# Kernel optimization log

Hardware: AMD Instinct MI355X
Metric: run time of the kernel (lower is better)

The kernel has to match this reference:

```python
import jax, jax.numpy as jnp
import numpy as np

CASCADES = 3
D, H, W = 64, 256, 256
HID = 8  # BasicBlock hidden channels


def fdiff(x, axis):
    """Forward difference D x along `axis` (last entry 0) == sparse dx/dy/dz matmul."""
    axis = axis % x.ndim
    pad = [(0, 0)] * x.ndim
    pad[axis] = (0, 1)
    return jnp.pad(jnp.diff(x, axis=axis), pad)


def fdiff_t(y, axis):
    """Exact transpose D^T y of fdiff: (D^T y)_0=-y_0, (D^T y)_j=y_{j-1}-y_j, (D^T y)_{n-1}=y_{n-2}."""
    axis = axis % y.ndim
    n = y.shape[axis]
    yl = jax.lax.slice_in_dim(y, 0, n - 1, axis=axis)  # y[0..n-2]
    pf = [(0, 0)] * y.ndim; pf[axis] = (1, 0)
    pb = [(0, 0)] * y.ndim; pb[axis] = (0, 1)
    return jnp.pad(yl, pf) - jnp.pad(yl, pb)


def conv3d(x, w, b):
    out = jax.lax.conv_general_dilated(
        x, w, window_strides=(1, 1, 1), padding='SAME',
        dimension_numbers=('NCDHW', 'OIDHW', 'NCDHW'))
    return out + b[None, :, None, None, None]


def basic_block(x, w1, b1, w2, b2):
    h = jax.nn.relu(conv3d(x, w1, b1))
    return conv3d(h, w2, b2), jnp.mean(jnp.abs(h))


def ite(t, sino):
    """BeijingGeometry stand-in: one SIRT-style step A^T(sino - A t)/D, A = sum over depth."""
    proj = jnp.sum(t, axis=2)               # [B,1,H,W]
    res = sino - proj
    return jnp.broadcast_to(res[:, :, None], t.shape) / t.shape[2]


def setup_inputs() -> dict:
    key = jax.random.key(0)
    ks = jax.random.split(key, 8)
    image = jax.random.normal(ks[0], (1, 1, D, H, W), dtype=jnp.float32)
    sino = jax.random.normal(ks[1], (1, 1, H, W), dtype=jnp.float32)
    # 4 BasicBlocks stacked on leading axis
    W1 = jax.random.normal(ks[2], (4, HID, 1, 3, 3, 3), dtype=jnp.float32) * 0.1
    B1 = jnp.zeros((4, HID), dtype=jnp.float32)
    W2 = jax.random.normal(ks[3], (4, 1, HID, 3, 3, 3), dtype=jnp.float32) * 0.1
    B2 = jnp.zeros((4, 1), dtype=jnp.float32)
    ntx = jnp.full((CASCADES,), -0.01, dtype=jnp.float32)
    nty = jnp.full((CASCADES,), -0.01, dtype=jnp.float32)
    ntz = jnp.full((CASCADES,), -0.01, dtype=jnp.float32)
    nt = jnp.full((CASCADES,), -0.1, dtype=jnp.float32)
    return {"image": image, "sino": sino, "W1": W1, "B1": B1, "W2": W2, "B2": B2,
            "ntx": ntx, "nty": nty, "ntz": ntz, "nt": nt}


def reference(image, sino, W1, B1, W2, B2, ntx, nty, ntz, nt):
    t = image
    p = q = s = jnp.float32(0.0)
    outs = [image]
    for c in range(CASCADES):
        z = t + ite(t, sino)
        pnew, _ = basic_block(fdiff(z, -1), W1[0], B1[0], W2[0], B2[0])  # d/dx (W axis)
        qnew, _ = basic_block(fdiff(z, -2), W1[1], B1[1], W2[1], B2[1])  # d/dy (H axis)
        snew, _ = basic_block(fdiff(z, -3), W1[2], B1[2], W2[2], B2[2])  # d/dz (D axis)
        znew, _ = basic_block(z, W1[3], B1[3], W2[3], B2[3])
        p = p + ntx[c] * (p - pnew)
        q = q + nty[c] * (q - qnew)
        s = s + ntz[c] * (s - snew)
        z_ = t + nt[c] * (t - znew)
        t = fdiff_t(p, -1) + fdiff_t(q, -2) + fdiff_t(s, -3) + z_
        outs.append(t)
    return jnp.stack(outs, axis=0)  # [cascades+1, B, 1, D, H, W]
```

## Files before the change

kernel.cpp:

```cpp
#include <hip/hip_runtime.h>

#define DD 64
#define HH 256
#define WW 256
#define HW (HH * WW)
#define NVOX (DD * HW)

#define TS 32
#define DR 36
#define HPH 40
#define CHB 16
#define NPF 6

typedef __fp16 half2v __attribute__((ext_vector_type(2)));

__global__ __launch_bounds__(256) void k_corr(const float* __restrict__ t,
                                              const float* __restrict__ sino,
                                              float* __restrict__ corr) {
  int idx = blockIdx.x * 256 + threadIdx.x;
  float s = 0.f;
#pragma unroll 8
  for (int d = 0; d < DD; ++d) s += t[d * HW + idx];
  corr[idx] = (sino[idx] - s) * (1.0f / DD);
}

__global__ __launch_bounds__(256, 4) void k_blocks(
    const float* __restrict__ t, const float* __restrict__ corr,
    float* __restrict__ p, float* __restrict__ q, float* __restrict__ s_,
    float* __restrict__ zb,
    const float* __restrict__ W1g, const float* __restrict__ B1g,
    const float* __restrict__ W2g, const float* __restrict__ B2g,
    const float* __restrict__ ntx, const float* __restrict__ nty,
    const float* __restrict__ ntz, const float* __restrict__ nt, int c) {
  __shared__ __align__(16) float dbuf[3][DR][DR];
  __shared__ __align__(16) __fp16 hbuf[8][34][HPH];

  const int b = blockIdx.z & 3;
  const int D0 = (blockIdx.z >> 2) * CHB;
  const int Dend = (D0 + CHB < DD) ? (D0 + CHB) : DD;
  const int ty0 = blockIdx.y * TS;
  const int tx0 = blockIdx.x * TS;
  const int tid = threadIdx.x;

  const float* w1 = W1g + b * 216;
  const float* w2 = W2g + b * 216;
  float b1[8];
#pragma unroll
  for (int ch = 0; ch < 8; ++ch) b1[ch] = B1g[b * 8 + ch];
  const float b2 = B2g[b];
  const float coef = (b == 0) ? ntx[c] : (b == 1) ? nty[c] : (b == 2) ? ntz[c] : nt[c];
  const float* prevBuf = (b == 0) ? p : (b == 1) ? q : (b == 2) ? s_ : t;
  float* outBuf = (b == 0) ? p : (b == 1) ? q : (b == 2) ? s_ : zb;
  const bool zeroPrev = (c == 0) && (b < 3);
  const int strideA = (b == 0) ? 1 : (b == 1) ? WW : HW;

  auto dslot = [](int f) { return (f + 6) % 3; };

  int cbt[NPF];
  float dC[NPF];
  unsigned mbits = 0;
#pragma unroll
  for (int k = 0; k < NPF; ++k) {
    int i = tid + k * 256;
    int iy = i / DR, ix = i - iy * DR;
    int gy = ty0 - 2 + iy, gx = tx0 - 2 + ix;
    bool inb = (i < DR * DR) && ((unsigned)gy < HH) && ((unsigned)gx < WW);
    int cb = gy * WW + gx;
    cbt[k] = cb;
    bool m;
    float d = 0.f;
    if (b == 0) {
      m = inb && (gx + 1 < WW);
      if (m) d = corr[cb + 1] - corr[cb];
    } else if (b == 1) {
      m = inb && (gy + 1 < HH);
      if (m) d = corr[cb + WW] - corr[cb];
    } else if (b == 2) {
      m = inb;
    } else {
      m = inb;
      if (m) d = corr[cb];
    }
    dC[k] = d;
    if (m) mbits |= (1u << k);
  }

  float pA0[NPF], pA1[NPF];

  auto issue_loads = [&](int f) {
    const bool fok = (f >= 0) && (f < DD) && (b != 2 || (f + 1 < DD));
    const int fb = f * HW;
#pragma unroll
    for (int k = 0; k < NPF; ++k) {
      pA0[k] = 0.f; pA1[k] = 0.f;
      if (fok && ((mbits >> k) & 1u)) {
        const float* base = t + fb + cbt[k];
        pA0[k] = base[0];
        if (b != 3) pA1[k] = base[strideA];
      }
    }
  };
  auto write_deriv = [&](int f) {
    float* dst = &dbuf[dslot(f)][0][0];
#pragma unroll
    for (int k = 0; k < NPF; ++k) {
      if (k < 5 || tid < (DR * DR - 5 * 256)) {
        float v = (b == 3) ? (pA0[k] + dC[k]) : ((pA1[k] - pA0[k]) + dC[k]);
        dst[tid + k * 256] = v;
      }
    }
  };

  auto conv1_patch = [&](const float* d0, const float* d1, const float* d2,
                         int jy, int jx, int ch0, int ch1) {
    float win[3][4][4];
#pragma unroll
    for (int r = 0; r < 4; ++r) {
      int off = (jy + r) * DR + jx;
      const float2* r0 = (const float2*)(d0 + off);
      const float2* r1 = (const float2*)(d1 + off);
      const float2* r2 = (const float2*)(d2 + off);
      float2 a, bb;
      a = r0[0]; bb = r0[1];
      win[0][r][0] = a.x; win[0][r][1] = a.y; win[0][r][2] = bb.x; win[0][r][3] = bb.y;
      a = r1[0]; bb = r1[1];
      win[1][r][0] = a.x; win[1][r][1] = a.y; win[1][r][2] = bb.x; win[1][r][3] = bb.y;
      a = r2[0]; bb = r2[1];
      win[2][r][0] = a.x; win[2][r][1] = a.y; win[2][r][2] = bb.x; win[2][r][3] = bb.y;
    }
    int gy0 = ty0 - 1 + jy, gx0 = tx0 - 1 + jx;
    bool in00 = ((unsigned)gy0 < HH) && ((unsigned)gx0 < WW);
    bool in01 = ((unsigned)gy0 < HH) && ((unsigned)(gx0 + 1) < WW);
    bool in10 = ((unsigned)(gy0 + 1) < HH) && ((unsigned)gx0 < WW);
    bool in11 = ((unsigned)(gy0 + 1) < HH) && ((unsigned)(gx0 + 1) < WW);
#pragma unroll 2
    for (int ch = ch0; ch < ch1; ++ch) {
      float bia = b1[ch];
      float a00 = bia, a01 = bia, a10 = bia, a11 = bia;
      const float* wch = w1 + ch * 27;
#pragma unroll
      for (int kz = 0; kz < 3; ++kz)
#pragma unroll
        for (int ky = 0; ky < 3; ++ky)
#pragma unroll
          for (int kx = 0; kx < 3; ++kx) {
            float wv = wch[kz * 9 + ky * 3 + kx];
            a00 = fmaf(wv, win[kz][ky][kx], a00);
            a01 = fmaf(wv, win[kz][ky][kx + 1], a01);
            a10 = fmaf(wv, win[kz][ky + 1][kx], a10);
            a11 = fmaf(wv, win[kz][ky + 1][kx + 1], a11);
          }
      half2v h0, h1;
      h0.x = (__fp16)(in00 ? fmaxf(a00, 0.f) : 0.f);
      h0.y = (__fp16)(in01 ? fmaxf(a01, 0.f) : 0.f);
      h1.x = (__fp16)(in10 ? fmaxf(a10, 0.f) : 0.f);
      h1.y = (__fp16)(in11 ? fmaxf(a11, 0.f) : 0.f);
      *(half2v*)&hbuf[ch][jy][jx] = h0;
      *(half2v*)&hbuf[ch][jy + 1][jx] = h1;
    }
  };

  auto comp_hidden = [&](int e) {
    const float* d0 = &dbuf[dslot(e - 1)][0][0];
    const float* d1 = &dbuf[dslot(e)][0][0];
    const float* d2 = &dbuf[dslot(e + 1)][0][0];
    {
      int prr = tid / 17, pcc = tid - prr * 17;
      conv1_patch(d0, d1, d2, prr * 2, pcc * 2, 0, 8);
    }
    if (tid < 132) {
      int m = tid >> 2, chp = (tid & 3) << 1;
      int pi = 256 + m;
      int prr = pi / 17, pcc = pi - prr * 17;
      conv1_patch(d0, d1, d2, prr * 2, pcc * 2, chp, chp + 2);
    }
  };

  const int txi = tid & 15, tyi = tid >> 4;
  const int px0 = txi * 2, py0 = tyi * 2;

  float aM[2][2], aC[2][2], aP[2][2];
#pragma unroll
  for (int i = 0; i < 2; ++i)
#pragma unroll
    for (int j = 0; j < 2; ++j) { aM[i][j] = b2; aC[i][j] = b2; aP[i][j] = b2; }

  issue_loads(D0 - 2); write_deriv(D0 - 2);
  issue_loads(D0 - 1); write_deriv(D0 - 1);
  issue_loads(D0);     write_deriv(D0);
  __syncthreads();

  for (int e = D0 - 1; e <= Dend; ++e) {
    const bool live = (e >= 0 && e < DD);
    issue_loads(e + 2);
    float2 pr0, pr1;
    pr0.x = pr0.y = pr1.x = pr1.y = 0.f;
    const int d = e - 1;
    const bool doStore = (e >= D0 + 1);
    if (doStore && !zeroPrev) {
      size_t v0 = (size_t)d * HW + (size_t)(ty0 + py0) * WW + tx0 + px0;
      pr0 = *(const float2*)&prevBuf[v0];
      pr1 = *(const float2*)&prevBuf[v0 + WW];
    }
    if (live) comp_hidden(e);
    __syncthreads();
    if (live) {
#pragma unroll 1
      for (int ch = 0; ch < 8; ++ch) {
        float hwf[4][4];
#pragma unroll
        for (int r = 0; r < 4; ++r) {
          const __fp16* hp = &hbuf[ch][py0 + r][px0];
          half2v a0 = *(const half2v*)hp;
          half2v a1 = *(const half2v*)(hp + 2);
          hwf[r][0] = (float)a0.x; hwf[r][1] = (float)a0.y;
          hwf[r][2] = (float)a1.x; hwf[r][3] = (float)a1.y;
        }
        const float* wch = w2 + ch * 27;
#pragma unroll
        for (int ky = 0; ky < 3; ++ky)
#pragma unroll
          for (int kx = 0; kx < 3; ++kx) {
            float w0 = wch[0 + ky * 3 + kx];
            float w1v = wch[9 + ky * 3 + kx];
            float w2v = wch[18 + ky * 3 + kx];
#pragma unroll
            for (int i = 0; i < 2; ++i)
#pragma unroll
              for (int j = 0; j < 2; ++j) {
                float h = hwf[i + ky][j + kx];
                aP[i][j] = fmaf(w0, h, aP[i][j]);
                aC[i][j] = fmaf(w1v, h, aC[i][j]);
                aM[i][j] = fmaf(w2v, h, aM[i][j]);
              }
          }
      }
    }
    write_deriv(e + 2);
    if (doStore) {
      size_t v0 = (size_t)d * HW + (size_t)(ty0 + py0) * WW + tx0 + px0;
      float2 o0, o1;
      o0.x = pr0.x + coef * (pr0.x - aM[0][0]);
      o0.y = pr0.y + coef * (pr0.y - aM[0][1]);
      o1.x = pr1.x + coef * (pr1.x - aM[1][0]);
      o1.y = pr1.y + coef * (pr1.y - aM[1][1]);
      *(float2*)&outBuf[v0] = o0;
      *(float2*)&outBuf[v0 + WW] = o1;
    }
#pragma unroll
    for (int i = 0; i < 2; ++i)
#pragma unroll
      for (int j = 0; j < 2; ++j) {
        aM[i][j] = aC[i][j]; aC[i][j] = aP[i][j]; aP[i][j] = b2;
      }
    __syncthreads();
  }
}

__global__ __launch_bounds__(256) void k_combine(
    const float* __restrict__ p, const float* __restrict__ q,
    const float* __restrict__ s_, const float* __restrict__ zb,
    float* __restrict__ tn) {
  int idx = blockIdx.x * 256 + threadIdx.x;
  int x = idx & (WW - 1);
  int y = (idx >> 8) & (HH - 1);
  int d = idx >> 16;
  float v = zb[idx];
  v += (x > 0 ? p[idx - 1] : 0.f) - (x < WW - 1 ? p[idx] : 0.f);
  v += (y > 0 ? q[idx - WW] : 0.f) - (y < HH - 1 ? q[idx] : 0.f);
  v += (d > 0 ? s_[idx - HW] : 0.f) - (d < DD - 1 ? s_[idx] : 0.f);
  tn[idx] = v;
}

extern "C" void kernel_launch(void* const* d_in, const int* in_sizes, int n_in,
                              void* d_out, int out_size, void* d_ws, size_t ws_size,
                              hipStream_t stream) {
  const float* image = (const float*)d_in[0];
  const float* sino  = (const float*)d_in[1];
  const float* W1    = (const float*)d_in[2];
  const float* B1    = (const float*)d_in[3];
  const float* W2    = (const float*)d_in[4];
  const float* B2    = (const float*)d_in[5];
  const float* ntx   = (const float*)d_in[6];
  const float* nty   = (const float*)d_in[7];
  const float* ntz   = (const float*)d_in[8];
  const float* nt    = (const float*)d_in[9];
  float* out = (float*)d_out;

  float* corr = (float*)d_ws;
  float* p  = corr + HW;
  float* q  = p + NVOX;
  float* s_ = q + NVOX;
  float* zb = s_ + NVOX;

  hipMemcpyAsync(out, image, (size_t)NVOX * sizeof(float),
                 hipMemcpyDeviceToDevice, stream);

  for (int c = 0; c < 3; ++c) {
    const float* t = out + (size_t)c * NVOX;
    float* tn = out + (size_t)(c + 1) * NVOX;
    k_corr<<<HW / 256, 256, 0, stream>>>(t, sino, corr);
    k_blocks<<<dim3(WW / TS, HH / TS, 16), 256, 0, stream>>>(
        t, corr, p, q, s_, zb, W1, B1, W2, B2, ntx, nty, ntz, nt, c);
    k_combine<<<NVOX / 256, 256, 0, stream>>>(p, q, s_, zb, tn);
  }
}
```

Measured before the change: 942.0 us.

## Process two depth planes per iteration with packed fp16 dot conv2

Restructures the fused conv kernel so each iteration computes hidden activations and second-conv contributions for two depth planes at once. The two planes share a 4-plane derivative window, and each depth block doubles to 32 planes, which halves the grid depth and cuts halo recomputation. The second conv now uses packed fp16 dot products (fdot2) with fp16-packed weights held in shared memory. In-bounds masking is skipped for interior tiles. The cost is more shared memory and registers: the occupancy hint drops from 4 to 2 blocks, and fdot2 may change rounding.

```diff
diff --git a/kernel.cpp b/kernel.cpp
--- a/kernel.cpp
+++ b/kernel.cpp
@@ -9,10 +9,17 @@
 #define TS 32
 #define DR 36
 #define HPH 40
-#define CHB 16
+#define CHB2 32
 #define NPF 6
 
 typedef __fp16 half2v __attribute__((ext_vector_type(2)));
+
+#if __has_builtin(__builtin_amdgcn_fdot2)
+#define FDOT2(a, b, c) __builtin_amdgcn_fdot2((a), (b), (c), false)
+#else
+#define FDOT2(a, b, c) \
+  fmaf((float)(a).x, (float)(b).x, fmaf((float)(a).y, (float)(b).y, (c)))
+#endif
 
 __global__ __launch_bounds__(256) void k_corr(const float* __restrict__ t,
                                               const float* __restrict__ sino,
@@ -24,7 +31,7 @@
   corr[idx] = (sino[idx] - s) * (1.0f / DD);
 }
 
-__global__ __launch_bounds__(256, 4) void k_blocks(
+__global__ __launch_bounds__(256, 2) void k_blocks(
     const float* __restrict__ t, const float* __restrict__ corr,
     float* __restrict__ p, float* __restrict__ q, float* __restrict__ s_,
     float* __restrict__ zb,
@@ -32,15 +39,16 @@
     const float* __restrict__ W2g, const float* __restrict__ B2g,
     const float* __restrict__ ntx, const float* __restrict__ nty,
     const float* __restrict__ ntz, const float* __restrict__ nt, int c) {
-  __shared__ __align__(16) float dbuf[3][DR][DR];
-  __shared__ __align__(16) __fp16 hbuf[8][34][HPH];
+  __shared__ __align__(16) float dbuf[4][DR][DR];
+  __shared__ __align__(16) __fp16 hbuf[2][8][34][HPH];
+  __shared__ __align__(8) half2v wpkl[72];
 
   const int b = blockIdx.z & 3;
-  const int D0 = (blockIdx.z >> 2) * CHB;
-  const int Dend = (D0 + CHB < DD) ? (D0 + CHB) : DD;
+  const int D0 = (blockIdx.z >> 2) * CHB2;
   const int ty0 = blockIdx.y * TS;
   const int tx0 = blockIdx.x * TS;
   const int tid = threadIdx.x;
+  const bool edgeT = (ty0 == 0) || (ty0 == HH - TS) || (tx0 == 0) || (tx0 == WW - TS);
 
   const float* w1 = W1g + b * 216;
   const float* w2 = W2g + b * 216;
@@ -54,7 +62,16 @@
   const bool zeroPrev = (c == 0) && (b < 3);
   const int strideA = (b == 0) ? 1 : (b == 1) ? WW : HW;
 
-  auto dslot = [](int f) { return (f + 6) % 3; };
+  auto dsl = [](int f) { return (f + 8) & 3; };
+
+  if (tid < 72) {
+    int ch = tid / 9, pr = tid - ch * 9;
+    const float* w = w2 + ch * 27 + pr * 3;
+    half2v hv;
+    hv.x = (__fp16)w[0];
+    hv.y = (__fp16)w[1];
+    wpkl[tid] = hv;
+  }
 
   int cbt[NPF];
   float dC[NPF];
@@ -85,58 +102,65 @@
     if (m) mbits |= (1u << k);
   }
 
-  float pA0[NPF], pA1[NPF];
-
-  auto issue_loads = [&](int f) {
+  float pA0a[NPF], pA1a[NPF], pA0b[NPF], pA1b[NPF];
+
+  auto issue_one = [&](int f, float (&A0)[NPF], float (&A1)[NPF]) {
     const bool fok = (f >= 0) && (f < DD) && (b != 2 || (f + 1 < DD));
     const int fb = f * HW;
 #pragma unroll
     for (int k = 0; k < NPF; ++k) {
-      pA0[k] = 0.f; pA1[k] = 0.f;
+      A0[k] = 0.f; A1[k] = 0.f;
       if (fok && ((mbits >> k) & 1u)) {
         const float* base = t + fb + cbt[k];
-        pA0[k] = base[0];
-        if (b != 3) pA1[k] = base[strideA];
+        A0[k] = base[0];
+        if (b != 3) A1[k] = base[strideA];
       }
     }
   };
-  auto write_deriv = [&](int f) {
-    float* dst = &dbuf[dslot(f)][0][0];
+  auto write_one = [&](int f, float (&A0)[NPF], float (&A1)[NPF]) {
+    float* dst = &dbuf[dsl(f)][0][0];
 #pragma unroll
     for (int k = 0; k < NPF; ++k) {
       if (k < 5 || tid < (DR * DR - 5 * 256)) {
-        float v = (b == 3) ? (pA0[k] + dC[k]) : ((pA1[k] - pA0[k]) + dC[k]);
+        float v = (b == 3) ? (A0[k] + dC[k]) : ((A1[k] - A0[k]) + dC[k]);
         dst[tid + k * 256] = v;
       }
     }
   };
 
-  auto conv1_patch = [&](const float* d0, const float* d1, const float* d2,
-                         int jy, int jx, int ch0, int ch1) {
-    float win[3][4][4];
+  auto conv1_pair = [&](const float* d0, const float* d1, const float* d2,
+                        const float* d3, int jy, int jx, int ch0, int ch1) {
+    float win[4][4][4];
 #pragma unroll
     for (int r = 0; r < 4; ++r) {
       int off = (jy + r) * DR + jx;
-      const float2* r0 = (const float2*)(d0 + off);
-      const float2* r1 = (const float2*)(d1 + off);
-      const float2* r2 = (const float2*)(d2 + off);
+      const float2* q0 = (const float2*)(d0 + off);
+      const float2* q1 = (const float2*)(d1 + off);
+      const float2* q2 = (const float2*)(d2 + off);
+      const float2* q3 = (const float2*)(d3 + off);
       float2 a, bb;
-      a = r0[0]; bb = r0[1];
+      a = q0[0]; bb = q0[1];
       win[0][r][0] = a.x; win[0][r][1] = a.y; win[0][r][2] = bb.x; win[0][r][3] = bb.y;
-      a = r1[0]; bb = r1[1];
+      a = q1[0]; bb = q1[1];
       win[1][r][0] = a.x; win[1][r][1] = a.y; win[1][r][2] = bb.x; win[1][r][3] = bb.y;
-      a = r2[0]; bb = r2[1];
+      a = q2[0]; bb = q2[1];
       win[2][r][0] = a.x; win[2][r][1] = a.y; win[2][r][2] = bb.x; win[2][r][3] = bb.y;
-    }
-    int gy0 = ty0 - 1 + jy, gx0 = tx0 - 1 + jx;
-    bool in00 = ((unsigned)gy0 < HH) && ((unsigned)gx0 < WW);
-    bool in01 = ((unsigned)gy0 < HH) && ((unsigned)(gx0 + 1) < WW);
-    bool in10 = ((unsigned)(gy0 + 1) < HH) && ((unsigned)gx0 < WW);
-    bool in11 = ((unsigned)(gy0 + 1) < HH) && ((unsigned)(gx0 + 1) < WW);
+      a = q3[0]; bb = q3[1];
+      win[3][r][0] = a.x; win[3][r][1] = a.y; win[3][r][2] = bb.x; win[3][r][3] = bb.y;
+    }
+    bool in00 = true, in01 = true, in10 = true, in11 = true;
+    if (edgeT) {
+      int gy0 = ty0 - 1 + jy, gx0 = tx0 - 1 + jx;
+      in00 = ((unsigned)gy0 < HH) && ((unsigned)gx0 < WW);
+      in01 = ((unsigned)gy0 < HH) && ((unsigned)(gx0 + 1) < WW);
+      in10 = ((unsigned)(gy0 + 1) < HH) && ((unsigned)gx0 < WW);
+      in11 = ((unsigned)(gy0 + 1) < HH) && ((unsigned)(gx0 + 1) < WW);
+    }
 #pragma unroll 2
     for (int ch = ch0; ch < ch1; ++ch) {
       float bia = b1[ch];
-      float a00 = bia, a01 = bia, a10 = bia, a11 = bia;
+      float aA00 = bia, aA01 = bia, aA10 = bia, aA11 = bia;
+      float aB00 = bia, aB01 = bia, aB10 = bia, aB11 = bia;
       const float* wch = w1 + ch * 27;
 #pragma unroll
       for (int kz = 0; kz < 3; ++kz)
@@ -145,116 +169,169 @@
 #pragma unroll
           for (int kx = 0; kx < 3; ++kx) {
             float wv = wch[kz * 9 + ky * 3 + kx];
-            a00 = fmaf(wv, win[kz][ky][kx], a00);
-            a01 = fmaf(wv, win[kz][ky][kx + 1], a01);
-            a10 = fmaf(wv, win[kz][ky + 1][kx], a10);
-            a11 = fmaf(wv, win[kz][ky + 1][kx + 1], a11);
+            aA00 = fmaf(wv, win[kz][ky][kx], aA00);
+            aA01 = fmaf(wv, win[kz][ky][kx + 1], aA01);
+            aA10 = fmaf(wv, win[kz][ky + 1][kx], aA10);
+            aA11 = fmaf(wv, win[kz][ky + 1][kx + 1], aA11);
+            aB00 = fmaf(wv, win[kz + 1][ky][kx], aB00);
+            aB01 = fmaf(wv, win[kz + 1][ky][kx + 1], aB01);
+            aB10 = fmaf(wv, win[kz + 1][ky + 1][kx], aB10);
+            aB11 = fmaf(wv, win[kz + 1][ky + 1][kx + 1], aB11);
           }
-      half2v h0, h1;
-      h0.x = (__fp16)(in00 ? fmaxf(a00, 0.f) : 0.f);
-      h0.y = (__fp16)(in01 ? fmaxf(a01, 0.f) : 0.f);
-      h1.x = (__fp16)(in10 ? fmaxf(a10, 0.f) : 0.f);
-      h1.y = (__fp16)(in11 ? fmaxf(a11, 0.f) : 0.f);
-      *(half2v*)&hbuf[ch][jy][jx] = h0;
-      *(half2v*)&hbuf[ch][jy + 1][jx] = h1;
+      float rA00 = fmaxf(aA00, 0.f), rA01 = fmaxf(aA01, 0.f);
+      float rA10 = fmaxf(aA10, 0.f), rA11 = fmaxf(aA11, 0.f);
+      float rB00 = fmaxf(aB00, 0.f), rB01 = fmaxf(aB01, 0.f);
+      float rB10 = fmaxf(aB10, 0.f), rB11 = fmaxf(aB11, 0.f);
+      if (edgeT) {
+        rA00 = in00 ? rA00 : 0.f; rA01 = in01 ? rA01 : 0.f;
+        rA10 = in10 ? rA10 : 0.f; rA11 = in11 ? rA11 : 0.f;
+        rB00 = in00 ? rB00 : 0.f; rB01 = in01 ? rB01 : 0.f;
+        rB10 = in10 ? rB10 : 0.f; rB11 = in11 ? rB11 : 0.f;
+      }
+      *(half2v*)&hbuf[0][ch][jy][jx]     = __builtin_amdgcn_cvt_pkrtz(rA00, rA01);
+      *(half2v*)&hbuf[0][ch][jy + 1][jx] = __builtin_amdgcn_cvt_pkrtz(rA10, rA11);
+      *(half2v*)&hbuf[1][ch][jy][jx]     = __builtin_amdgcn_cvt_pkrtz(rB00, rB01);
+      *(half2v*)&hbuf[1][ch][jy + 1][jx] = __builtin_amdgcn_cvt_pkrtz(rB10, rB11);
     }
   };
 
-  auto comp_hidden = [&](int e) {
-    const float* d0 = &dbuf[dslot(e - 1)][0][0];
-    const float* d1 = &dbuf[dslot(e)][0][0];
-    const float* d2 = &dbuf[dslot(e + 1)][0][0];
+  auto comp_hidden_pair = [&](int e) {
+    const float* d0 = &dbuf[dsl(e - 1)][0][0];
+    const float* d1 = &dbuf[dsl(e)][0][0];
+    const float* d2 = &dbuf[dsl(e + 1)][0][0];
+    const float* d3 = &dbuf[dsl(e + 2)][0][0];
     {
       int prr = tid / 17, pcc = tid - prr * 17;
-      conv1_patch(d0, d1, d2, prr * 2, pcc * 2, 0, 8);
+      conv1_pair(d0, d1, d2, d3, prr * 2, pcc * 2, 0, 8);
     }
     if (tid < 132) {
       int m = tid >> 2, chp = (tid & 3) << 1;
       int pi = 256 + m;
       int prr = pi / 17, pcc = pi - prr * 17;
-      conv1_patch(d0, d1, d2, prr * 2, pcc * 2, chp, chp + 2);
+      conv1_pair(d0, d1, d2, d3, prr * 2, pcc * 2, chp, chp + 2);
     }
   };
 
   const int txi = tid & 15, tyi = tid >> 4;
   const int px0 = txi * 2, py0 = tyi * 2;
 
-  float aM[2][2], aC[2][2], aP[2][2];
+  float A0_[2][2], A1_[2][2], A2_[2][2], A3_[2][2];
 #pragma unroll
   for (int i = 0; i < 2; ++i)
 #pragma unroll
-    for (int j = 0; j < 2; ++j) { aM[i][j] = b2; aC[i][j] = b2; aP[i][j] = b2; }
-
-  issue_loads(D0 - 2); write_deriv(D0 - 2);
-  issue_loads(D0 - 1); write_deriv(D0 - 1);
-  issue_loads(D0);     write_deriv(D0);
+    for (int j = 0; j < 2; ++j) {
+      A0_[i][j] = b2; A1_[i][j] = b2; A2_[i][j] = b2; A3_[i][j] = b2;
+    }
+
+  issue_one(D0 - 2, pA0a, pA1a); issue_one(D0 - 1, pA0b, pA1b);
+  write_one(D0 - 2, pA0a, pA1a); write_one(D0 - 1, pA0b, pA1b);
+  issue_one(D0,     pA0a, pA1a); issue_one(D0 + 1, pA0b, pA1b);
+  write_one(D0,     pA0a, pA1a); write_one(D0 + 1, pA0b, pA1b);
   __syncthreads();
 
-  for (int e = D0 - 1; e <= Dend; ++e) {
-    const bool live = (e >= 0 && e < DD);
-    issue_loads(e + 2);
-    float2 pr0, pr1;
-    pr0.x = pr0.y = pr1.x = pr1.y = 0.f;
-    const int d = e - 1;
-    const bool doStore = (e >= D0 + 1);
+#define CONV2_PLANE(PL, AP, AC, AM)                                          \
+  {                                                                          \
+    half2v H0[4], HPv[4];                                                    \
+    float c0[4], c1[4];                                                      \
+    _Pragma("unroll")                                                        \
+    for (int r = 0; r < 4; ++r) {                                            \
+      const __fp16* hp = &hbuf[PL][ch][py0 + r][px0];                        \
+      half2v h0 = *(const half2v*)hp;                                        \
+      half2v h1 = *(const half2v*)(hp + 2);                                  \
+      unsigned u0, u1;                                                       \
+      __builtin_memcpy(&u0, &h0, 4);                                         \
+      __builtin_memcpy(&u1, &h1, 4);                                         \
+      unsigned pm = (u1 << 16) | (u0 >> 16);                                 \
+      half2v hpv;                                                            \
+      __builtin_memcpy(&hpv, &pm, 4);                                        \
+      H0[r] = h0; HPv[r] = hpv;                                              \
+      c0[r] = (float)h1.x; c1[r] = (float)h1.y;                              \
+    }                                                                        \
+    _Pragma("unroll")                                                        \
+    for (int ky = 0; ky < 3; ++ky)                                           \
+      _Pragma("unroll")                                                      \
+      for (int i = 0; i < 2; ++i) {                                          \
+        const int r = i + ky;                                                \
+        const half2v hE = H0[r], hO = HPv[r];                                \
+        const float s0v = c0[r], s1v = c1[r];                                \
+        {                                                                    \
+          half2v wv = wrow[ky]; float ws = wch[ky * 3 + 2];                  \
+          AP[i][0] = FDOT2(hE, wv, AP[i][0]);                                \
+          AP[i][0] = fmaf(ws, s0v, AP[i][0]);                                \
+          AP[i][1] = FDOT2(hO, wv, AP[i][1]);                                \
+          AP[i][1] = fmaf(ws, s1v, AP[i][1]);                                \
+        }                                                                    \
+        {                                                                    \
+          half2v wv = wrow[3 + ky]; float ws = wch[9 + ky * 3 + 2];          \
+          AC[i][0] = FDOT2(hE, wv, AC[i][0]);                                \
+          AC[i][0] = fmaf(ws, s0v, AC[i][0]);                                \
+          AC[i][1] = FDOT2(hO, wv, AC[i][1]);                                \
+          AC[i][1] = fmaf(ws, s1v, AC[i][1]);                                \
+        }                                                                    \
+        {                                                                    \
+          half2v wv = wrow[6 + ky]; float ws = wch[18 + ky * 3 + 2];         \
+          AM[i][0] = FDOT2(hE, wv, AM[i][0]);                                \
+          AM[i][0] = fmaf(ws, s0v, AM[i][0]);                                \
+          AM[i][1] = FDOT2(hO, wv, AM[i][1]);                                \
+          AM[i][1] = fmaf(ws, s1v, AM[i][1]);                                \
+        }                                                                    \
+      }                                                                      \
+  }
+
+  for (int k = 0; k < 17; ++k) {
+    const int e = D0 - 1 + 2 * k;
+    const bool liveA = (e >= 0);
+    const bool liveB = (e + 1 < DD);
+    issue_one(e + 3, pA0a, pA1a);
+    issue_one(e + 4, pA0b, pA1b);
+    const bool doStore = (k >= 1);
+    float2 prA0, prA1, prB0, prB1;
+    prA0.x = prA0.y = prA1.x = prA1.y = 0.f;
+    prB0.x = prB0.y = prB1.x = prB1.y = 0.f;
     if (doStore && !zeroPrev) {
-      size_t v0 = (size_t)d * HW + (size_t)(ty0 + py0) * WW + tx0 + px0;
-      pr0 = *(const float2*)&prevBuf[v0];
-      pr1 = *(const float2*)&prevBuf[v0 + WW];
-    }
-    if (live) comp_hidden(e);
+      size_t v0 = (size_t)(e - 1) * HW + (size_t)(ty0 + py0) * WW + tx0 + px0;
+      prA0 = *(const float2*)&prevBuf[v0];
+      prA1 = *(const float2*)&prevBuf[v0 + WW];
+      prB0 = *(const float2*)&prevBuf[v0 + HW];
+      prB1 = *(const float2*)&prevBuf[v0 + HW + WW];
+    }
+    comp_hidden_pair(e);
     __syncthreads();
-    if (live) {
 #pragma unroll 1
-      for (int ch = 0; ch < 8; ++ch) {
-        float hwf[4][4];
-#pragma unroll
-        for (int r = 0; r < 4; ++r) {
-          const __fp16* hp = &hbuf[ch][py0 + r][px0];
-          half2v a0 = *(const half2v*)hp;
-          half2v a1 = *(const half2v*)(hp + 2);
-          hwf[r][0] = (float)a0.x; hwf[r][1] = (float)a0.y;
-          hwf[r][2] = (float)a1.x; hwf[r][3] = (float)a1.y;
-        }
-        const float* wch = w2 + ch * 27;
-#pragma unroll
-        for (int ky = 0; ky < 3; ++ky)
-#pragma unroll
-          for (int kx = 0; kx < 3; ++kx) {
-            float w0 = wch[0 + ky * 3 + kx];
-            float w1v = wch[9 + ky * 3 + kx];
-            float w2v = wch[18 + ky * 3 + kx];
-#pragma unroll
-            for (int i = 0; i < 2; ++i)
-#pragma unroll
-              for (int j = 0; j < 2; ++j) {
-                float h = hwf[i + ky][j + kx];
-                aP[i][j] = fmaf(w0, h, aP[i][j]);
-                aC[i][j] = fmaf(w1v, h, aC[i][j]);
-                aM[i][j] = fmaf(w2v, h, aM[i][j]);
-              }
-          }
-      }
-    }
-    write_deriv(e + 2);
+    for (int ch = 0; ch < 8; ++ch) {
+      const float* wch = w2 + ch * 27;
+      const half2v* wrow = &wpkl[ch * 9];
+      if (liveA) CONV2_PLANE(0, A2_, A1_, A0_);
+      if (liveB) CONV2_PLANE(1, A3_, A2_, A1_);
+    }
+    write_one(e + 3, pA0a, pA1a);
+    write_one(e + 4, pA0b, pA1b);
     if (doStore) {
-      size_t v0 = (size_t)d * HW + (size_t)(ty0 + py0) * WW + tx0 + px0;
-      float2 o0, o1;
-      o0.x = pr0.x + coef * (pr0.x - aM[0][0]);
-      o0.y = pr0.y + coef * (pr0.y - aM[0][1]);
-      o1.x = pr1.x + coef * (pr1.x - aM[1][0]);
-      o1.y = pr1.y + coef * (pr1.y - aM[1][1]);
-      *(float2*)&outBuf[v0] = o0;
-      *(float2*)&outBuf[v0 + WW] = o1;
+      size_t v0 = (size_t)(e - 1) * HW + (size_t)(ty0 + py0) * WW + tx0 + px0;
+      float2 o;
+      o.x = prA0.x + coef * (prA0.x - A0_[0][0]);
+      o.y = prA0.y + coef * (prA0.y - A0_[0][1]);
+      *(float2*)&outBuf[v0] = o;
+      o.x = prA1.x + coef * (prA1.x - A0_[1][0]);
+      o.y = prA1.y + coef * (prA1.y - A0_[1][1]);
+      *(float2*)&outBuf[v0 + WW] = o;
+      o.x = prB0.x + coef * (prB0.x - A1_[0][0]);
+      o.y = prB0.y + coef * (prB0.y - A1_[0][1]);
+      *(float2*)&outBuf[v0 + HW] = o;
+      o.x = prB1.x + coef * (prB1.x - A1_[1][0]);
+      o.y = prB1.y + coef * (prB1.y - A1_[1][1]);
+      *(float2*)&outBuf[v0 + HW + WW] = o;
     }
 #pragma unroll
     for (int i = 0; i < 2; ++i)
 #pragma unroll
       for (int j = 0; j < 2; ++j) {
-        aM[i][j] = aC[i][j]; aC[i][j] = aP[i][j]; aP[i][j] = b2;
+        A0_[i][j] = A2_[i][j]; A1_[i][j] = A3_[i][j];
+        A2_[i][j] = b2;        A3_[i][j] = b2;
       }
     __syncthreads();
   }
+#undef CONV2_PLANE
 }
 
 __global__ __launch_bounds__(256) void k_combine(
@@ -300,7 +377,7 @@
     const float* t = out + (size_t)c * NVOX;
     float* tn = out + (size_t)(c + 1) * NVOX;
     k_corr<<<HW / 256, 256, 0, stream>>>(t, sino, corr);
-    k_blocks<<<dim3(WW / TS, HH / TS, 16), 256, 0, stream>>>(
+    k_blocks<<<dim3(WW / TS, HH / TS, 8), 256, 0, stream>>>(
         t, corr, p, q, s_, zb, W1, B1, W2, B2, ntx, nty, ntz, nt, c);
     k_combine<<<NVOX / 256, 256, 0, stream>>>(p, q, s_, zb, tn);
   }
```

New measurement: 1.010 ms. 7.2% more time.
